# Performance work log

Hardware: AMD Instinct MI355X
Metric: run time of the kernel (lower is better)

The kernel has to match this reference:

```python
import jax, jax.numpy as jnp
import numpy as np
from jax import lax

S = 1024  # input_size
G = 10    # grid_size
F = 5     # fiter_size -> 11x11 gaussian kernel
B = 8
C = 3


def _gauss(size, fwhm):
    x = np.arange(size, dtype=np.float64)
    y = x[:, None]
    c = size // 2
    g = np.exp(-4 * np.log(2) * ((x - c) ** 2 + (y - c) ** 2) / fwhm ** 2)
    return (g / g.sum()).astype(np.float32)


def setup_inputs() -> dict:
    key = jax.random.key(0)
    k1, k2, k3 = jax.random.split(key, 3)
    x = jax.random.normal(k1, (B, C, S, S), dtype=jnp.float32)
    offset_x = jax.random.normal(k2, (B, 1, G, G), dtype=jnp.float32)
    offset_y = jax.random.normal(k3, (B, 1, G, G), dtype=jnp.float32)
    weight = jnp.asarray(_gauss(2 * F + 1, F))[None, None]  # [1,1,11,11]
    return {"x": x, "offset_x": offset_x, "offset_y": offset_y,
            "weight": weight, "max_move": 50}


def reference(x, offset_x, offset_y, weight, max_move):
    max_offset = 2.0 * max_move / S

    def smooth(o):  # replication pad + 11x11 gaussian conv + scale + clamp
        p = jnp.pad(o, ((0, 0), (0, 0), (F, F), (F, F)), mode="edge")
        c = lax.conv_general_dilated(p, weight, (1, 1), "VALID",
                                     dimension_numbers=("NCHW", "OIHW", "NCHW"))
        return jnp.clip(c * max_offset, -max_offset, max_offset)

    g = jnp.concatenate([smooth(offset_x), smooth(offset_y)], axis=1)  # [B,2,G,G]

    # bilinear upsample G -> S (align_corners=False, like F.interpolate)
    src = jnp.maximum((jnp.arange(S, dtype=jnp.float32) + 0.5) * (G / S) - 0.5, 0.0)
    i0 = jnp.minimum(jnp.floor(src).astype(jnp.int32), G - 1)
    i1 = jnp.minimum(i0 + 1, G - 1)
    w = src - i0.astype(jnp.float32)
    g = g[:, :, i0, :] * (1 - w)[None, None, :, None] + g[:, :, i1, :] * w[None, None, :, None]
    g = g[:, :, :, i0] * (1 - w) + g[:, :, :, i1] * w  # [B,2,S,S]

    # P basis: channel 0 = x coord, channel 1 = y coord, scaled to [-1,1]
    lin = jnp.arange(S, dtype=jnp.float32) / (S - 1.0)
    P = jnp.stack([jnp.broadcast_to(lin[None, :], (S, S)),
                   jnp.broadcast_to(lin[:, None], (S, S))]) * 2.0 - 1.0
    grid = jnp.clip(g + P, -1.0, 1.0).transpose(0, 2, 3, 1)  # [B,S,S,2] (x,y)

    def gs(img, gr):  # grid_sample bilinear, zeros padding, align_corners=False
        ix = ((gr[..., 0] + 1.0) * S - 1.0) / 2.0
        iy = ((gr[..., 1] + 1.0) * S - 1.0) / 2.0
        x0 = jnp.floor(ix).astype(jnp.int32); x1 = x0 + 1
        y0 = jnp.floor(iy).astype(jnp.int32); y1 = y0 + 1
        wx = ix - x0.astype(ix.dtype)
        wy = iy - y0.astype(iy.dtype)

        def corner(yy, xx, wt):
            v = img[:, jnp.clip(yy, 0, S - 1), jnp.clip(xx, 0, S - 1)]  # [C,S,S]
            m = ((yy >= 0) & (yy < S) & (xx >= 0) & (xx < S)).astype(img.dtype)
            return v * (m * wt)

        return (corner(y0, x0, (1 - wy) * (1 - wx)) + corner(y0, x1, (1 - wy) * wx)
                + corner(y1, x0, wy * (1 - wx)) + corner(y1, x1, wy * wx))

    return jax.vmap(gs)(x, grid)
```

## Files before the change

kernel.cpp:

```cpp
#include <hip/hip_runtime.h>

#define SS 1024
#define GG 10
#define FF 5
#define BB 8
#define CC 3
#define KK (2 * FF + 1)

__global__ __launch_bounds__(256) void rds_smooth_kernel(
    const float* __restrict__ ox, const float* __restrict__ oy,
    const float* __restrict__ w, const void* __restrict__ max_move_p,
    float* __restrict__ gs)
{
    int idx = blockIdx.x * 256 + threadIdx.x;
    if (idx >= BB * 2 * GG * GG) return;
    int j  = idx % GG;
    int i  = (idx / GG) % GG;
    int ch = (idx / (GG * GG)) % 2;
    int b  = idx / (2 * GG * GG);

    const float* o = (ch == 0 ? ox : oy) + b * GG * GG;

    int mi = *(const int*)max_move_p;
    float mv = (mi >= -100000 && mi <= 100000) ? (float)mi : __int_as_float(mi);
    float max_offset = 2.0f * mv / (float)SS;

    float acc = 0.0f;
    for (int u = 0; u < KK; ++u) {
        int yy = min(max(i + u - FF, 0), GG - 1);
        for (int v = 0; v < KK; ++v) {
            int xx = min(max(j + v - FF, 0), GG - 1);
            acc += o[yy * GG + xx] * w[u * KK + v];
        }
    }
    acc *= max_offset;
    acc = fminf(fmaxf(acc, -max_offset), max_offset);
    gs[idx] = acc;
}

__global__ __launch_bounds__(256, 4) void rds_deform_kernel(
    const float* __restrict__ x, const float* __restrict__ gs,
    float* __restrict__ out)
{
    int bx    = blockIdx.x;
    int xseg  = bx & 3;
    int ytile = (bx >> 2) & 255;
    int b     = bx >> 10;
    int tid   = threadIdx.x;
    int ybase = ytile << 2;
    int xc    = (xseg << 8) + tid;

    __shared__ float rowf[4][2][GG];

    const float GdS = (float)GG / (float)SS;

    if (tid < 80) {
        int p  = tid / 20;
        int r  = tid - p * 20;
        int ch = r / GG;
        int j  = r - ch * GG;
        int y  = ybase + p;
        float sy  = fmaxf(((float)y + 0.5f) * GdS - 0.5f, 0.0f);
        int   i0y = min((int)sy, GG - 1);
        int   i1y = min(i0y + 1, GG - 1);
        float wyu = sy - (float)i0y;
        const float* gb = gs + (b * 2 + ch) * GG * GG;
        rowf[p][ch][j] = gb[i0y * GG + j] + wyu * (gb[i1y * GG + j] - gb[i0y * GG + j]);
    }
    __syncthreads();

    float sx  = fmaxf(((float)xc + 0.5f) * GdS - 0.5f, 0.0f);
    int   i0x = min((int)sx, GG - 1);
    int   i1x = min(i0x + 1, GG - 1);
    float wxu = sx - (float)i0x;
    float pxc = (float)xc * (2.0f / (float)(SS - 1)) - 1.0f;

    int   o00[4], o01[4], o10[4], o11[4];
    float w00[4], w01[4], w10[4], w11[4];

    #pragma unroll
    for (int p = 0; p < 4; ++p) {
        float r0a = rowf[p][0][i0x], r0b = rowf[p][0][i1x];
        float r1a = rowf[p][1][i0x], r1b = rowf[p][1][i1x];
        float gxv = r0a + wxu * (r0b - r0a);
        float gyv = r1a + wxu * (r1b - r1a);

        float py  = (float)(ybase + p) * (2.0f / (float)(SS - 1)) - 1.0f;
        float gr0 = fminf(fmaxf(gxv + pxc, -1.0f), 1.0f);
        float gr1 = fminf(fmaxf(gyv + py,  -1.0f), 1.0f);

        float ix = gr0 * 512.0f + 511.5f;
        float iy = gr1 * 512.0f + 511.5f;

        int   x0 = (int)floorf(ix);
        int   x1 = x0 + 1;
        int   y0 = (int)floorf(iy);
        int   y1 = y0 + 1;
        float wx = ix - (float)x0;
        float wy = iy - (float)y0;

        float mx0 = ((unsigned)x0 < (unsigned)SS) ? 1.0f : 0.0f;
        float mx1 = ((unsigned)x1 < (unsigned)SS) ? 1.0f : 0.0f;
        float my0 = ((unsigned)y0 < (unsigned)SS) ? 1.0f : 0.0f;
        float my1 = ((unsigned)y1 < (unsigned)SS) ? 1.0f : 0.0f;

        w00[p] = (1.0f - wy) * (1.0f - wx) * my0 * mx0;
        w01[p] = (1.0f - wy) * wx          * my0 * mx1;
        w10[p] = wy          * (1.0f - wx) * my1 * mx0;
        w11[p] = wy          * wx          * my1 * mx1;

        int cx0 = min(max(x0, 0), SS - 1);
        int cx1 = min(max(x1, 0), SS - 1);
        int cy0 = min(max(y0, 0), SS - 1);
        int cy1 = min(max(y1, 0), SS - 1);

        o00[p] = cy0 * SS + cx0;
        o01[p] = cy0 * SS + cx1;
        o10[p] = cy1 * SS + cx0;
        o11[p] = cy1 * SS + cx1;
    }

    const float* xb = x + (size_t)b * CC * SS * SS;
    size_t obase = (((size_t)b * CC) * SS + ybase) * SS + xc;

    #pragma unroll
    for (int c = 0; c < CC; ++c) {
        const float* img = xb + (size_t)c * SS * SS;
        float v[4];
        #pragma unroll
        for (int p = 0; p < 4; ++p) {
            v[p] = img[o00[p]] * w00[p] + img[o01[p]] * w01[p]
                 + img[o10[p]] * w10[p] + img[o11[p]] * w11[p];
        }
        #pragma unroll
        for (int p = 0; p < 4; ++p) {
            out[obase + (size_t)c * SS * SS + (size_t)(p * SS)] = v[p];
        }
    }
}

extern "C" void kernel_launch(void* const* d_in, const int* in_sizes, int n_in,
                              void* d_out, int out_size, void* d_ws, size_t ws_size,
                              hipStream_t stream) {
    const float* x        = (const float*)d_in[0];
    const float* offset_x = (const float*)d_in[1];
    const float* offset_y = (const float*)d_in[2];
    const float* weight   = (const float*)d_in[3];
    const void*  max_move = d_in[4];
    float* out = (float*)d_out;
    float* gs  = (float*)d_ws;

    int n1 = BB * 2 * GG * GG;
    rds_smooth_kernel<<<(n1 + 255) / 256, 256, 0, stream>>>(
        offset_x, offset_y, weight, max_move, gs);

    int nblocks = BB * (SS / 4) * 4;
    rds_deform_kernel<<<nblocks, 256, 0, stream>>>(x, gs, out);
}
```

Baseline: 206.6 us.

## Load horizontal texel pairs as float2, batch all gathers, use nontemporal stores

The kernel now fetches each pair of horizontally adjacent texels with a single 8-byte load, using a clamped base column and remapped x-weights to keep edge handling correct. All gathers for all channels and rows are issued up front behind a scheduling barrier to raise memory-level parallelism. Output writes become nontemporal stores to avoid polluting cache. This halves the number of load instructions and increases overlap, at the cost of higher register pressure from holding 24 float2 values per thread.

```diff
diff --git a/kernel.cpp b/kernel.cpp
--- a/kernel.cpp
+++ b/kernel.cpp
@@ -6,6 +6,8 @@
 #define BB 8
 #define CC 3
 #define KK (2 * FF + 1)
+
+typedef float f32x2 __attribute__((ext_vector_type(2), aligned(4)));
 
 __global__ __launch_bounds__(256) void rds_smooth_kernel(
     const float* __restrict__ ox, const float* __restrict__ oy,
@@ -75,8 +77,9 @@
     float wxu = sx - (float)i0x;
     float pxc = (float)xc * (2.0f / (float)(SS - 1)) - 1.0f;
 
-    int   o00[4], o01[4], o10[4], o11[4];
-    float w00[4], w01[4], w10[4], w11[4];
+    int   oa[4], ob[4];
+    float wxa[4], wxb[4];
+    float wya[4], wyb[4];
 
     #pragma unroll
     for (int p = 0; p < 4; ++p) {
@@ -93,48 +96,52 @@
         float iy = gr1 * 512.0f + 511.5f;
 
         int   x0 = (int)floorf(ix);
-        int   x1 = x0 + 1;
         int   y0 = (int)floorf(iy);
         int   y1 = y0 + 1;
         float wx = ix - (float)x0;
         float wy = iy - (float)y0;
 
-        float mx0 = ((unsigned)x0 < (unsigned)SS) ? 1.0f : 0.0f;
-        float mx1 = ((unsigned)x1 < (unsigned)SS) ? 1.0f : 0.0f;
+        int base = min(max(x0, 0), SS - 2);
+        int d    = x0 - base;
+        wxa[p] = (d == 0) ? (1.0f - wx) : ((d < 0) ? wx : 0.0f);
+        wxb[p] = (d == 0) ? wx          : ((d < 0) ? 0.0f : (1.0f - wx));
+
         float my0 = ((unsigned)y0 < (unsigned)SS) ? 1.0f : 0.0f;
         float my1 = ((unsigned)y1 < (unsigned)SS) ? 1.0f : 0.0f;
+        wya[p] = (1.0f - wy) * my0;
+        wyb[p] = wy * my1;
 
-        w00[p] = (1.0f - wy) * (1.0f - wx) * my0 * mx0;
-        w01[p] = (1.0f - wy) * wx          * my0 * mx1;
-        w10[p] = wy          * (1.0f - wx) * my1 * mx0;
-        w11[p] = wy          * wx          * my1 * mx1;
-
-        int cx0 = min(max(x0, 0), SS - 1);
-        int cx1 = min(max(x1, 0), SS - 1);
         int cy0 = min(max(y0, 0), SS - 1);
         int cy1 = min(max(y1, 0), SS - 1);
-
-        o00[p] = cy0 * SS + cx0;
-        o01[p] = cy0 * SS + cx1;
-        o10[p] = cy1 * SS + cx0;
-        o11[p] = cy1 * SS + cx1;
+        oa[p] = cy0 * SS + base;
+        ob[p] = cy1 * SS + base;
     }
 
     const float* xb = x + (size_t)b * CC * SS * SS;
-    size_t obase = (((size_t)b * CC) * SS + ybase) * SS + xc;
 
+    f32x2 la[CC * 4], lb[CC * 4];
     #pragma unroll
     for (int c = 0; c < CC; ++c) {
         const float* img = xb + (size_t)c * SS * SS;
-        float v[4];
         #pragma unroll
         for (int p = 0; p < 4; ++p) {
-            v[p] = img[o00[p]] * w00[p] + img[o01[p]] * w01[p]
-                 + img[o10[p]] * w10[p] + img[o11[p]] * w11[p];
+            la[c * 4 + p] = *(const f32x2*)(img + oa[p]);
+            lb[c * 4 + p] = *(const f32x2*)(img + ob[p]);
         }
+    }
+    __builtin_amdgcn_sched_barrier(0);
+
+    size_t obase = (((size_t)b * CC) * SS + ybase) * SS + xc;
+    #pragma unroll
+    for (int c = 0; c < CC; ++c) {
         #pragma unroll
         for (int p = 0; p < 4; ++p) {
-            out[obase + (size_t)c * SS * SS + (size_t)(p * SS)] = v[p];
+            f32x2 fa = la[c * 4 + p];
+            f32x2 fb = lb[c * 4 + p];
+            float v = wya[p] * (fa.x * wxa[p] + fa.y * wxb[p])
+                    + wyb[p] * (fb.x * wxa[p] + fb.y * wxb[p]);
+            __builtin_nontemporal_store(
+                v, out + obase + (size_t)c * SS * SS + (size_t)(p * SS));
         }
     }
 }
```

Result: faster. 201.2 us (-2.6%).
